# Kernel tuning notes

Measured on AMD Instinct MI355X. Metric: run time of the kernel, lower is better.

Reference implementation:

```python
import jax, jax.numpy as jnp
import numpy as np

EPS = 1e-6  # config.model.train_hparams.eps
DIM_MODEL = 512
DIM_K = 64  # dim_q = dim_k = dim_v


def setup_inputs() -> dict:
    key = jax.random.key(0)
    ks = jax.random.split(key, 10)
    B, S = 8, 2048
    query = jax.random.normal(ks[0], (B, S, DIM_MODEL), dtype=jnp.float32)
    key_t = jax.random.normal(ks[1], (B, S, DIM_MODEL), dtype=jnp.float32)
    value = jax.random.normal(ks[2], (B, S, DIM_MODEL), dtype=jnp.float32)
    attention_mask = jax.random.randint(ks[3], (B, S, S), 0, 2, dtype=jnp.int32)
    lim = 1.0 / np.sqrt(DIM_MODEL)
    Wq = jax.random.uniform(ks[4], (DIM_K, DIM_MODEL), jnp.float32, -lim, lim)
    bq = jax.random.uniform(ks[5], (DIM_K,), jnp.float32, -lim, lim)
    Wk = jax.random.uniform(ks[6], (DIM_K, DIM_MODEL), jnp.float32, -lim, lim)
    bk = jax.random.uniform(ks[7], (DIM_K,), jnp.float32, -lim, lim)
    Wv = jax.random.uniform(ks[8], (DIM_K, DIM_MODEL), jnp.float32, -lim, lim)
    bv = jax.random.uniform(ks[9], (DIM_K,), jnp.float32, -lim, lim)
    return {"query": query, "key": key_t, "value": value,
            "attention_mask": attention_mask,
            "Wq": Wq, "bq": bq, "Wk": Wk, "bk": bk, "Wv": Wv, "bv": bv}


def reference(query, key, value, attention_mask, Wq, bq, Wk, bk, Wv, bv):
    scale = DIM_K ** (-0.5)
    q = jnp.einsum('bsm,dm->bsd', query, Wq) + bq   # (B,S,dk)
    k = jnp.einsum('bsm,dm->bsd', key, Wk) + bk
    v = jnp.einsum('bsm,dm->bsd', value, Wv) + bv
    qk = jnp.einsum('bqd,bkd->bqk', q, k) * scale   # (B,S,S)
    qk = jnp.where(qk == 0, EPS, qk)                 # masked_fill(qk == 0, eps)
    qk = jnp.where(attention_mask == 0, EPS, qk)     # masked_fill(mask == 0, eps)
    attention_weight = jax.nn.softmax(qk, axis=-1)
    attention = jnp.einsum('bqk,bkd->bqd', attention_weight, v)
    return attention, attention_weight
```

## Files before the change

### kernel.cpp

```cpp
#include <hip/hip_runtime.h>

#define BATCH 8
#define SEQ   2048
#define DM    512
#define DK    64
#define NROW  (BATCH*SEQ)
#define EPSV  1e-6f

typedef _Float16 f16x8 __attribute__((ext_vector_type(8)));
typedef _Float16 f16x4 __attribute__((ext_vector_type(4)));
typedef _Float16 f16x2 __attribute__((ext_vector_type(2)));
typedef float    f32x4 __attribute__((ext_vector_type(4)));

#define MFMA16(a,b,c) __builtin_amdgcn_mfma_f32_16x16x32_f16(a, b, c, 0, 0, 0)

__global__ void wcvt(const float* __restrict__ wq, const float* __restrict__ wk,
                     const float* __restrict__ wv, _Float16* __restrict__ w16) {
    int idx = (blockIdx.x * 256 + threadIdx.x) * 4;
    int z = idx >> 15;
    int off = idx & 32767;
    const float* src = (z == 0) ? wq : ((z == 1) ? wk : wv);
    float4 g = *reinterpret_cast<const float4*>(src + off);
    f16x4 h = { (_Float16)g.x, (_Float16)g.y, (_Float16)g.z, (_Float16)g.w };
    *reinterpret_cast<f16x4*>(w16 + idx) = h;
}

__global__ __launch_bounds__(256) void proj(
    const float* __restrict__ query, const float* __restrict__ key,
    const float* __restrict__ value, const _Float16* __restrict__ w16,
    const float* __restrict__ bq, const float* __restrict__ bk, const float* __restrict__ bv,
    _Float16* __restrict__ q16, _Float16* __restrict__ k16, _Float16* __restrict__ vT16)
{
    __shared__ _Float16 xsh[64][72];

    const int t = threadIdx.x;
    const int wave = t >> 6, lane = t & 63;
    const int n16 = lane & 15, quad = lane >> 4;
    const int z = blockIdx.y;
    const float* in   = (z == 0) ? query : ((z == 1) ? key : value);
    const float* bias = (z == 0) ? bq    : ((z == 1) ? bk  : bv);
    const _Float16* wz = w16 + z * (DK * DM);
    const int row0 = blockIdx.x * 64;

    f32x4 acc[4] = {};

    for (int kk = 0; kk < DM; kk += 64) {
        #pragma unroll
        for (int it = 0; it < 4; ++it) {
            int f = t + it * 256;
            int row = f >> 4, kq = f & 15;
            float4 g = *reinterpret_cast<const float4*>(in + (size_t)(row0 + row) * DM + kk + kq * 4);
            f16x4 h = { (_Float16)g.x, (_Float16)g.y, (_Float16)g.z, (_Float16)g.w };
            *reinterpret_cast<f16x4*>(&xsh[row][kq * 4]) = h;
        }
        __syncthreads();
        f16x8 a0 = *reinterpret_cast<const f16x8*>(&xsh[wave * 16 + n16][quad * 8]);
        f16x8 a1 = *reinterpret_cast<const f16x8*>(&xsh[wave * 16 + n16][32 + quad * 8]);
        #pragma unroll
        for (int nt = 0; nt < 4; ++nt) {
            const _Float16* bbase = wz + (size_t)(nt * 16 + n16) * DM + kk + quad * 8;
            f16x8 b0 = *reinterpret_cast<const f16x8*>(bbase);
            f16x8 b1 = *reinterpret_cast<const f16x8*>(bbase + 32);
            acc[nt] = MFMA16(a0, b0, acc[nt]);
            acc[nt] = MFMA16(a1, b1, acc[nt]);
        }
        __syncthreads();
    }

    const int batch = row0 >> 11, row0s = row0 & (SEQ - 1);
    if (z < 2) {
        _Float16* out = (z == 0) ? q16 : k16;
        #pragma unroll
        for (int nt = 0; nt < 4; ++nt) {
            float bzv = bias[nt * 16 + n16];
            #pragma unroll
            for (int r = 0; r < 4; ++r) {
                int grow = row0 + wave * 16 + quad * 4 + r;
                out[(size_t)grow * DK + nt * 16 + n16] = (_Float16)(acc[nt][r] + bzv);
            }
        }
    } else {
        #pragma unroll
        for (int nt = 0; nt < 4; ++nt) {
            float bzv = bias[nt * 16 + n16];
            #pragma unroll
            for (int r = 0; r < 4; ++r)
                xsh[nt * 16 + n16][wave * 16 + quad * 4 + r] = (_Float16)(acc[nt][r] + bzv);
        }
        __syncthreads();
        int d = t >> 2, s0 = (t & 3) * 16;
        _Float16* dst = vT16 + ((size_t)(batch * DK + d)) * SEQ + row0s + s0;
        f16x8 h0, h1;
        #pragma unroll
        for (int j = 0; j < 8; ++j) { h0[j] = xsh[d][s0 + j]; h1[j] = xsh[d][s0 + 8 + j]; }
        *reinterpret_cast<f16x8*>(dst)     = h0;
        *reinterpret_cast<f16x8*>(dst + 8) = h1;
    }
}

#define RT  16
#define SCH 2056

__global__ __launch_bounds__(512, 4) void attn(
    const _Float16* __restrict__ q16,
    const _Float16* __restrict__ k16,
    const _Float16* __restrict__ vT16,
    const int* __restrict__ mask,
    float* __restrict__ attno,
    float* __restrict__ aw)
{
    __shared__ _Float16 sc[RT][SCH];
    __shared__ float red[4][16][17];
    __shared__ float st_il[RT];

    const int t = threadIdx.x;
    const int wave = t >> 6, lane = t & 63;
    const int n16 = lane & 15, quad = lane >> 4;
    const int row0 = blockIdx.x * RT;
    const int batch = row0 >> 11, row0s = row0 & (SEQ - 1);

    {
        const _Float16* qb = q16 + (size_t)(row0 + n16) * DK + quad * 8;
        f16x8 aq0 = *reinterpret_cast<const f16x8*>(qb);
        f16x8 aq1 = *reinterpret_cast<const f16x8*>(qb + 32);
        const _Float16* kbase = k16 + (size_t)(batch * SEQ) * DK;
        const _Float16* kb = kbase + (size_t)(wave * 16 + n16) * DK + quad * 8;
        f16x8 b0 = *reinterpret_cast<const f16x8*>(kb);
        f16x8 b1 = *reinterpret_cast<const f16x8*>(kb + 32);
        for (int c = 0; c < 16; ++c) {
            f16x8 cb0 = b0, cb1 = b1;
            if (c < 15) {
                const _Float16* nb = kbase + (size_t)((c + 1) * 128 + wave * 16 + n16) * DK + quad * 8;
                b0 = *reinterpret_cast<const f16x8*>(nb);
                b1 = *reinterpret_cast<const f16x8*>(nb + 32);
            }
            f32x4 acc = {};
            acc = MFMA16(aq0, cb0, acc);
            acc = MFMA16(aq1, cb1, acc);
            int col = c * 128 + wave * 16 + n16;
            #pragma unroll
            for (int r = 0; r < 4; ++r)
                sc[quad * 4 + r][col] = (_Float16)(acc[r] * 0.125f);
        }
    }
    __syncthreads();

    #pragma unroll 1
    for (int rr = 0; rr < 2; ++rr) {
        int row = wave * 2 + rr;
        const int4* mrow = reinterpret_cast<const int4*>(
            mask + (size_t)batch * SEQ * SEQ + (size_t)(row0s + row) * SEQ);
        float e[32];
        float vmax = -3.4e38f;
        #pragma unroll
        for (int it = 0; it < 8; ++it) {
            int j = it * 64 + lane;
            int4  m4 = mrow[j];
            f16x4 s4 = *reinterpret_cast<const f16x4*>(&sc[row][j * 4]);
            float s0 = (float)s4[0], s1 = (float)s4[1], s2 = (float)s4[2], s3 = (float)s4[3];
            s0 = (m4.x == 0 || s0 == 0.0f) ? EPSV : s0;
            s1 = (m4.y == 0 || s1 == 0.0f) ? EPSV : s1;
            s2 = (m4.z == 0 || s2 == 0.0f) ? EPSV : s2;
            s3 = (m4.w == 0 || s3 == 0.0f) ? EPSV : s3;
            e[it * 4 + 0] = s0; e[it * 4 + 1] = s1; e[it * 4 + 2] = s2; e[it * 4 + 3] = s3;
            vmax = fmaxf(vmax, fmaxf(fmaxf(s0, s1), fmaxf(s2, s3)));
        }
        #pragma unroll
        for (int off = 32; off; off >>= 1) vmax = fmaxf(vmax, __shfl_xor(vmax, off));
        float vsum = 0.0f;
        #pragma unroll
        for (int it = 0; it < 8; ++it) {
            int j = it * 64 + lane;
            float e0 = __expf(e[it * 4 + 0] - vmax), e1 = __expf(e[it * 4 + 1] - vmax);
            float e2 = __expf(e[it * 4 + 2] - vmax), e3 = __expf(e[it * 4 + 3] - vmax);
            e[it * 4 + 0] = e0; e[it * 4 + 1] = e1; e[it * 4 + 2] = e2; e[it * 4 + 3] = e3;
            f16x4 h = { (_Float16)e0, (_Float16)e1, (_Float16)e2, (_Float16)e3 };
            *reinterpret_cast<f16x4*>(&sc[row][j * 4]) = h;
            vsum += (e0 + e1) + (e2 + e3);
        }
        #pragma unroll
        for (int off = 32; off; off >>= 1) vsum += __shfl_xor(vsum, off);
        float il = 1.0f / vsum;
        if (lane == 0) st_il[row] = il;
        float* awrow = aw + (size_t)batch * SEQ * SEQ + (size_t)(row0s + row) * SEQ;
        #pragma unroll
        for (int it = 0; it < 8; ++it) {
            int j = it * 64 + lane;
            float4 p4 = { e[it * 4 + 0] * il, e[it * 4 + 1] * il,
                          e[it * 4 + 2] * il, e[it * 4 + 3] * il };
            *reinterpret_cast<float4*>(awrow + j * 4) = p4;
        }
    }
    __syncthreads();

    {
        const int dblk = wave & 3, khalf = wave >> 2;
        f32x4 oacc = {};
        const _Float16* vbase = vT16 + ((size_t)(batch * DK + dblk * 16 + n16)) * SEQ
                              + khalf * 1024;
        const _Float16* scrow = &sc[n16][khalf * 1024];
        f16x8 bv0 = *reinterpret_cast<const f16x8*>(vbase + quad * 8);
        f16x8 bv1 = *reinterpret_cast<const f16x8*>(vbase + 32 + quad * 8);
        for (int c = 0; c < 16; ++c) {
            f16x8 cb0 = bv0, cb1 = bv1;
            if (c < 15) {
                bv0 = *reinterpret_cast<const f16x8*>(vbase + (c + 1) * 64 + quad * 8);
                bv1 = *reinterpret_cast<const f16x8*>(vbase + (c + 1) * 64 + 32 + quad * 8);
            }
            f16x8 a0 = *reinterpret_cast<const f16x8*>(scrow + c * 64 + quad * 8);
            f16x8 a1 = *reinterpret_cast<const f16x8*>(scrow + c * 64 + 32 + quad * 8);
            oacc = MFMA16(a0, cb0, oacc);
            oacc = MFMA16(a1, cb1, oacc);
        }
        if (khalf == 1) {
            #pragma unroll
            for (int r = 0; r < 4; ++r)
                red[dblk][quad * 4 + r][n16] = oacc[r];
        }
        __syncthreads();
        if (khalf == 0) {
            #pragma unroll
            for (int r = 0; r < 4; ++r) {
                int row = quad * 4 + r;
                float o = oacc[r] + red[dblk][row][n16];
                attno[(size_t)(row0 + row) * DK + dblk * 16 + n16] = o * st_il[row];
            }
        }
    }
}

extern "C" void kernel_launch(void* const* d_in, const int* in_sizes, int n_in,
                              void* d_out, int out_size, void* d_ws, size_t ws_size,
                              hipStream_t stream) {
    const float* query = (const float*)d_in[0];
    const float* key   = (const float*)d_in[1];
    const float* value = (const float*)d_in[2];
    const int*   amask = (const int*)d_in[3];
    const float* Wq = (const float*)d_in[4];
    const float* bq = (const float*)d_in[5];
    const float* Wk = (const float*)d_in[6];
    const float* bk = (const float*)d_in[7];
    const float* Wv = (const float*)d_in[8];
    const float* bv = (const float*)d_in[9];

    float* attno = (float*)d_out;
    float* aw    = attno + (size_t)NROW * DK;

    char* ws = (char*)d_ws;
    _Float16* q16  = (_Float16*)(ws);
    _Float16* k16  = (_Float16*)(ws + (size_t)2097152);
    _Float16* vT16 = (_Float16*)(ws + (size_t)4194304);
    _Float16* w16  = (_Float16*)(ws + (size_t)6291456);

    wcvt<<<96, 256, 0, stream>>>(Wq, Wk, Wv, w16);
    proj<<<dim3(NROW / 64, 3), 256, 0, stream>>>(query, key, value, w16,
                                                 bq, bk, bv, q16, k16, vT16);
    attn<<<NROW / RT, 512, 0, stream>>>(q16, k16, vT16, amask, attno, aw);
}
```

Before: 377.2 us.

## Load projection inputs directly to registers and stage softmax values in LDS

The projection kernel stops staging input tiles through shared memory with barriers. Each lane now loads its own fp32 A-fragment straight from global memory, prefetching the next k-chunk in registers. The softmax drops its 32-float per-thread register array and instead writes the masked scores and exponentials back into the fp16 shared score buffer, rereading them for each pass. This is meant to cut register pressure and barrier overhead, at the cost of extra LDS traffic and fp16 rounding of the scores before the max and exp steps.

```diff
diff --git a/kernel.cpp b/kernel.cpp
--- a/kernel.cpp
+++ b/kernel.cpp
@@ -9,7 +9,6 @@
 
 typedef _Float16 f16x8 __attribute__((ext_vector_type(8)));
 typedef _Float16 f16x4 __attribute__((ext_vector_type(4)));
-typedef _Float16 f16x2 __attribute__((ext_vector_type(2)));
 typedef float    f32x4 __attribute__((ext_vector_type(4)));
 
 #define MFMA16(a,b,c) __builtin_amdgcn_mfma_f32_16x16x32_f16(a, b, c, 0, 0, 0)
@@ -41,21 +40,27 @@
     const float* bias = (z == 0) ? bq    : ((z == 1) ? bk  : bv);
     const _Float16* wz = w16 + z * (DK * DM);
     const int row0 = blockIdx.x * 64;
+    const float* abase = in + (size_t)(row0 + wave * 16 + n16) * DM + quad * 8;
 
     f32x4 acc[4] = {};
 
+    float4 p0 = *reinterpret_cast<const float4*>(abase);
+    float4 p1 = *reinterpret_cast<const float4*>(abase + 4);
+    float4 p2 = *reinterpret_cast<const float4*>(abase + 32);
+    float4 p3 = *reinterpret_cast<const float4*>(abase + 36);
+
+    #pragma unroll 2
     for (int kk = 0; kk < DM; kk += 64) {
-        #pragma unroll
-        for (int it = 0; it < 4; ++it) {
-            int f = t + it * 256;
-            int row = f >> 4, kq = f & 15;
-            float4 g = *reinterpret_cast<const float4*>(in + (size_t)(row0 + row) * DM + kk + kq * 4);
-            f16x4 h = { (_Float16)g.x, (_Float16)g.y, (_Float16)g.z, (_Float16)g.w };
-            *reinterpret_cast<f16x4*>(&xsh[row][kq * 4]) = h;
-        }
-        __syncthreads();
-        f16x8 a0 = *reinterpret_cast<const f16x8*>(&xsh[wave * 16 + n16][quad * 8]);
-        f16x8 a1 = *reinterpret_cast<const f16x8*>(&xsh[wave * 16 + n16][32 + quad * 8]);
+        f16x8 a0 = { (_Float16)p0.x, (_Float16)p0.y, (_Float16)p0.z, (_Float16)p0.w,
+                     (_Float16)p1.x, (_Float16)p1.y, (_Float16)p1.z, (_Float16)p1.w };
+        f16x8 a1 = { (_Float16)p2.x, (_Float16)p2.y, (_Float16)p2.z, (_Float16)p2.w,
+                     (_Float16)p3.x, (_Float16)p3.y, (_Float16)p3.z, (_Float16)p3.w };
+        if (kk < DM - 64) {
+            p0 = *reinterpret_cast<const float4*>(abase + kk + 64);
+            p1 = *reinterpret_cast<const float4*>(abase + kk + 68);
+            p2 = *reinterpret_cast<const float4*>(abase + kk + 96);
+            p3 = *reinterpret_cast<const float4*>(abase + kk + 100);
+        }
         #pragma unroll
         for (int nt = 0; nt < 4; ++nt) {
             const _Float16* bbase = wz + (size_t)(nt * 16 + n16) * DM + kk + quad * 8;
@@ -64,7 +69,6 @@
             acc[nt] = MFMA16(a0, b0, acc[nt]);
             acc[nt] = MFMA16(a1, b1, acc[nt]);
         }
-        __syncthreads();
     }
 
     const int batch = row0 >> 11, row0s = row0 & (SEQ - 1);
@@ -150,7 +154,7 @@
         int row = wave * 2 + rr;
         const int4* mrow = reinterpret_cast<const int4*>(
             mask + (size_t)batch * SEQ * SEQ + (size_t)(row0s + row) * SEQ);
-        float e[32];
+
         float vmax = -3.4e38f;
         #pragma unroll
         for (int it = 0; it < 8; ++it) {
@@ -162,18 +166,20 @@
             s1 = (m4.y == 0 || s1 == 0.0f) ? EPSV : s1;
             s2 = (m4.z == 0 || s2 == 0.0f) ? EPSV : s2;
             s3 = (m4.w == 0 || s3 == 0.0f) ? EPSV : s3;
-            e[it * 4 + 0] = s0; e[it * 4 + 1] = s1; e[it * 4 + 2] = s2; e[it * 4 + 3] = s3;
+            f16x4 h = { (_Float16)s0, (_Float16)s1, (_Float16)s2, (_Float16)s3 };
+            *reinterpret_cast<f16x4*>(&sc[row][j * 4]) = h;
             vmax = fmaxf(vmax, fmaxf(fmaxf(s0, s1), fmaxf(s2, s3)));
         }
         #pragma unroll
         for (int off = 32; off; off >>= 1) vmax = fmaxf(vmax, __shfl_xor(vmax, off));
+
         float vsum = 0.0f;
         #pragma unroll
         for (int it = 0; it < 8; ++it) {
             int j = it * 64 + lane;
-            float e0 = __expf(e[it * 4 + 0] - vmax), e1 = __expf(e[it * 4 + 1] - vmax);
-            float e2 = __expf(e[it * 4 + 2] - vmax), e3 = __expf(e[it * 4 + 3] - vmax);
-            e[it * 4 + 0] = e0; e[it * 4 + 1] = e1; e[it * 4 + 2] = e2; e[it * 4 + 3] = e3;
+            f16x4 s4 = *reinterpret_cast<const f16x4*>(&sc[row][j * 4]);
+            float e0 = __expf((float)s4[0] - vmax), e1 = __expf((float)s4[1] - vmax);
+            float e2 = __expf((float)s4[2] - vmax), e3 = __expf((float)s4[3] - vmax);
             f16x4 h = { (_Float16)e0, (_Float16)e1, (_Float16)e2, (_Float16)e3 };
             *reinterpret_cast<f16x4*>(&sc[row][j * 4]) = h;
             vsum += (e0 + e1) + (e2 + e3);
@@ -182,12 +188,14 @@
         for (int off = 32; off; off >>= 1) vsum += __shfl_xor(vsum, off);
         float il = 1.0f / vsum;
         if (lane == 0) st_il[row] = il;
+
         float* awrow = aw + (size_t)batch * SEQ * SEQ + (size_t)(row0s + row) * SEQ;
         #pragma unroll
         for (int it = 0; it < 8; ++it) {
             int j = it * 64 + lane;
-            float4 p4 = { e[it * 4 + 0] * il, e[it * 4 + 1] * il,
-                          e[it * 4 + 2] * il, e[it * 4 + 3] * il };
+            f16x4 e4 = *reinterpret_cast<const f16x4*>(&sc[row][j * 4]);
+            float4 p4 = { (float)e4[0] * il, (float)e4[1] * il,
+                          (float)e4[2] * il, (float)e4[3] * il };
             *reinterpret_cast<float4*>(awrow + j * 4) = p4;
         }
     }
```

New measurement: 369.5 us. 1.02x faster.
